# Optimization experiments

Hardware: AMD Instinct MI355X
Metric: run time of the kernel (lower is better)

Reference implementation:

```python
import jax, jax.numpy as jnp
import numpy as np

ALPHA = 0.2          # LeakyReLU negative slope
NEG_INF = -9.0e15    # padding value used by the torch code before softmax


def setup_inputs() -> dict:
    key = jax.random.key(0)
    k1, k2, k3, k4 = jax.random.split(key, 4)
    B, N, F_IN, F_OUT = 32, 1024, 128, 128
    # Dense 0/1 adjacency with self-loops (every node has degree >= 1)
    u = jax.random.uniform(k1, (B, N, N))
    adj = (u < 0.03).astype(jnp.float32)
    adj = jnp.maximum(adj, jnp.eye(N, dtype=jnp.float32)[None, :, :])
    batch_features = jax.random.normal(k2, (B, N, F_IN), dtype=jnp.float32)
    W = jax.random.normal(k3, (F_OUT, F_IN), dtype=jnp.float32) * 0.1  # nn.Linear weight [out,in]
    a = jax.random.normal(k4, (2 * F_OUT, 1), dtype=jnp.float32) * 0.1
    return {"batch_graphs": adj, "batch_features": batch_features, "W": W, "a": a}


def reference(batch_graphs, batch_features, W, a):
    # batch_graphs: [B,N,N] 0/1 adjacency; batch_features: [B,N,F_in]
    D = W.shape[0]
    h = jnp.einsum('bnf,df->bnd', batch_features, W)  # fc (no bias), dropout=0 is a no-op
    # score(i,j) = LeakyReLU(a[:D].h_i + a[D:].h_j); concat order is [center_i || neighbor_j]
    a_src = a[:D, 0]
    a_dst = a[D:, 0]
    s = h @ a_src                                   # [B,N] center term
    t = h @ a_dst                                   # [B,N] neighbor term
    scores = s[:, :, None] + t[:, None, :]          # [B,N,N]
    scores = jnp.where(scores > 0, scores, ALPHA * scores)
    # segmented softmax over each node's neighbors (pad_sequence with -9e15 == masked softmax)
    masked = jnp.where(batch_graphs == 1.0, scores, NEG_INF)
    attn = jax.nn.softmax(masked, axis=-1) * batch_graphs  # *adj zeros non-edges exactly (and deg-0 rows)
    # weighted sum of neighbor features scattered back to each node
    out = jnp.einsum('bij,bjd->bid', attn, h)       # [B,N,D]
    return out
```

## Files before the change

kernel.cpp:

```cpp
#include <hip/hip_runtime.h>
#include <hip/hip_bf16.h>

#define B_ 32
#define N_ 1024
#define F_ 128
#define ALPHA_ 0.2f
#define PSTR 72

typedef __attribute__((ext_vector_type(8))) short short8_t;
typedef __attribute__((ext_vector_type(4))) short short4_t;
typedef __attribute__((ext_vector_type(4))) float f32x4;

static __device__ __forceinline__ unsigned short bf16b(float f) {
    return __bfloat16_as_ushort(__float2bfloat16(f));
}

#define WAIT_VM2()  asm volatile("s_waitcnt vmcnt(2)" ::: "memory")
#define WAIT_VM0()  asm volatile("s_waitcnt vmcnt(0)" ::: "memory")
#define WAIT_LGKM() asm volatile("s_waitcnt lgkmcnt(0)" ::: "memory")
#define SCHEDB()    __builtin_amdgcn_sched_barrier(0)
#define BAR()       __builtin_amdgcn_s_barrier()

__global__ __launch_bounds__(256) void hst_kernel(
    const float* __restrict__ feat, const float* __restrict__ W,
    const float* __restrict__ a, float* __restrict__ h,
    float* __restrict__ s_out, float* __restrict__ t_out)
{
    __shared__ unsigned short Wt[128 * 128];
    __shared__ float fl[64 * 128];
    const int tid = threadIdx.x;
    const long row0 = (long)blockIdx.x * 64;

    for (int i = tid; i < 128 * 128; i += 256) {
        int d = i >> 7, k = i & 127;
        Wt[k * 128 + d] = bf16b(W[i]);
    }
    for (int i = tid; i < 64 * 128; i += 256) {
        int r = i >> 7, k = i & 127;
        fl[r * 128 + ((k + 8 * (r >> 2)) & 127)] = feat[(row0 + r) * 128 + k];
    }
    __syncthreads();

    const int oct = tid & 15;
    const int rg  = tid >> 4;
    const int d0  = oct * 8;
    const int r0  = rg * 4;

    float acc[4][8];
    #pragma unroll
    for (int q = 0; q < 4; ++q)
        #pragma unroll
        for (int c = 0; c < 8; ++c) acc[q][c] = 0.f;

    for (int kc = 0; kc < 128; kc += 4) {
        float wv[4][8];
        #pragma unroll
        for (int kk = 0; kk < 4; ++kk) {
            short8_t wr = *reinterpret_cast<const short8_t*>(&Wt[(kc + kk) * 128 + d0]);
            #pragma unroll
            for (int c = 0; c < 8; ++c) {
                union { unsigned u; float f; } cv;
                cv.u = ((unsigned)(unsigned short)wr[c]) << 16;
                wv[kk][c] = cv.f;
            }
        }
        #pragma unroll
        for (int q = 0; q < 4; ++q) {
            int r = r0 + q;
            int koff = (kc + 8 * (r >> 2)) & 127;
            float4 fv = *reinterpret_cast<const float4*>(&fl[r * 128 + koff]);
            float fq[4] = {fv.x, fv.y, fv.z, fv.w};
            #pragma unroll
            for (int kk = 0; kk < 4; ++kk)
                #pragma unroll
                for (int c = 0; c < 8; ++c)
                    acc[q][c] = fmaf(fq[kk], wv[kk][c], acc[q][c]);
        }
    }

    float asrc[8], adst[8];
    #pragma unroll
    for (int c = 0; c < 8; ++c) { asrc[c] = a[d0 + c]; adst[c] = a[128 + d0 + c]; }

    #pragma unroll
    for (int q = 0; q < 4; ++q) {
        long row = row0 + r0 + q;
        float4 h0 = make_float4(acc[q][0], acc[q][1], acc[q][2], acc[q][3]);
        float4 h1 = make_float4(acc[q][4], acc[q][5], acc[q][6], acc[q][7]);
        *reinterpret_cast<float4*>(&h[row * 128 + d0])     = h0;
        *reinterpret_cast<float4*>(&h[row * 128 + d0 + 4]) = h1;
        float sv = 0.f, tv = 0.f;
        #pragma unroll
        for (int c = 0; c < 8; ++c) {
            sv = fmaf(acc[q][c], asrc[c], sv);
            tv = fmaf(acc[q][c], adst[c], tv);
        }
        #pragma unroll
        for (int off = 1; off < 16; off <<= 1) {
            sv += __shfl_xor(sv, off);
            tv += __shfl_xor(tv, off);
        }
        if (oct == 0) { s_out[row] = sv; t_out[row] = tv; }
    }
}

__global__ __launch_bounds__(256) void tr_kernel(
    const float* __restrict__ h, unsigned short* __restrict__ hT)
{
    __shared__ unsigned short lt[128 * PSTR];
    const int tid = threadIdx.x;
    const int b   = blockIdx.x >> 4;
    const int j0  = (blockIdx.x & 15) * 64;

    const int j  = tid >> 2;
    const int dc = (tid & 3) * 4;
    const float* hr = h + ((size_t)(b * N_ + j0 + j)) * F_;
    #pragma unroll
    for (int q = 0; q < 8; ++q) {
        float4 v = *reinterpret_cast<const float4*>(hr + dc + q * 16);
        #pragma unroll
        for (int e = 0; e < 4; ++e)
            lt[(dc + q * 16 + e) * PSTR + j] = bf16b((&v.x)[e]);
    }
    __syncthreads();

    const int d    = tid >> 1;
    const int half = tid & 1;
    unsigned short* dst = hT + ((size_t)b * F_ + d) * N_ + j0 + half * 32;
    #pragma unroll
    for (int q = 0; q < 4; ++q)
        *reinterpret_cast<short8_t*>(dst + q * 8) =
            *reinterpret_cast<const short8_t*>(&lt[d * PSTR + half * 32 + q * 8]);
}

__global__ __launch_bounds__(512, 4) void attn4_kernel(
    const float* __restrict__ adj, const unsigned short* __restrict__ hT,
    const float* __restrict__ s_in, const float* __restrict__ t_in,
    float* __restrict__ out)
{
    __shared__ float adjb[2][64 * 64];
    __shared__ unsigned short ht[128 * PSTR];
    __shared__ unsigned short pt[64 * PSTR];
    __shared__ float tl[N_];
    __shared__ float sl[64], rsl[64];

    const int tid  = threadIdx.x;
    const int lane = tid & 63;
    const int w    = tid >> 6;

    const int blk = (blockIdx.x & 7) * 64 + (blockIdx.x >> 3);
    const int b   = blk >> 4;
    const int i0  = (blk & 15) * 64;

    tl[tid]       = t_in[b * N_ + tid];
    tl[tid + 512] = t_in[b * N_ + tid + 512];
    if (tid < 64) sl[tid] = s_in[b * N_ + i0 + tid];

    const int sr = w * 8 + (lane >> 4);
    const int sc = (lane & 15) * 4;
    const float* gsrc = adj + (size_t)(b * N_ + i0) * N_;

#define STAGE_ADJ(K, BUF) do {                                                 \
    __builtin_amdgcn_global_load_lds(                                          \
        (const __attribute__((address_space(1))) void*)                        \
            (gsrc + (size_t)sr * N_ + (K) * 64 + sc),                          \
        (__attribute__((address_space(3))) void*)&adjb[BUF][(w * 2 + 0) * 256],\
        16, 0, 0);                                                             \
    __builtin_amdgcn_global_load_lds(                                          \
        (const __attribute__((address_space(1))) void*)                        \
            (gsrc + (size_t)(sr + 4) * N_ + (K) * 64 + sc),                    \
        (__attribute__((address_space(3))) void*)&adjb[BUF][(w * 2 + 1) * 256],\
        16, 0, 0);                                                             \
} while (0)

    const unsigned short* hTb = hT + (size_t)b * F_ * N_;
    short8_t h_reg[2];
#define LOAD_H(K) do {                                                         \
    _Pragma("unroll")                                                          \
    for (int c = 0; c < 2; ++c) {                                              \
        int ch = tid + c * 512;                                                \
        h_reg[c] = *reinterpret_cast<const short8_t*>(                         \
            hTb + (size_t)(ch >> 3) * N_ + ((K) * 64 + (ch & 7) * 8));         \
    }                                                                          \
} while (0)

    const int gi = tid >> 3;
    const int gj = (tid & 7) * 8;
    const int m0 = (w >> 2) * 32;
    const int n0 = (w & 3) * 32;
    const int lm = tid & 15;
    const int kg = (tid & 63) >> 4;

    f32x4 acc[2][2];
    #pragma unroll
    for (int nf = 0; nf < 2; ++nf)
        #pragma unroll
        for (int mf = 0; mf < 2; ++mf) acc[nf][mf] = (f32x4){0.f, 0.f, 0.f, 0.f};
    float rs = 0.f;

    STAGE_ADJ(0, 0);
    LOAD_H(0);
    WAIT_VM2();
    WAIT_LGKM();
    SCHEDB();
    BAR();
    const float s_i = sl[gi];

    #pragma unroll
    for (int k = 0; k < 16; ++k) {
        const int cur = k & 1;
        if (k + 1 < 16) STAGE_ADJ(k + 1, cur ^ 1);
        #pragma unroll
        for (int c = 0; c < 2; ++c) {
            int ch = tid + c * 512;
            *reinterpret_cast<short8_t*>(&ht[(ch >> 3) * PSTR + (ch & 7) * 8]) = h_reg[c];
        }
        {
            float4 a0 = *reinterpret_cast<const float4*>(&adjb[cur][gi * 64 + gj]);
            float4 a1 = *reinterpret_cast<const float4*>(&adjb[cur][gi * 64 + gj + 4]);
            float4 t0 = *reinterpret_cast<const float4*>(&tl[k * 64 + gj]);
            float4 t1 = *reinterpret_cast<const float4*>(&tl[k * 64 + gj + 4]);
            short4_t pk0, pk1;
            #pragma unroll
            for (int e = 0; e < 4; ++e) {
                float sc0 = s_i + (&t0.x)[e];
                sc0 = fmaxf(sc0, ALPHA_ * sc0);
                float p = __expf(sc0) * (&a0.x)[e];
                rs += p;
                pk0[e] = (short)bf16b(p);
            }
            #pragma unroll
            for (int e = 0; e < 4; ++e) {
                float sc1 = s_i + (&t1.x)[e];
                sc1 = fmaxf(sc1, ALPHA_ * sc1);
                float p = __expf(sc1) * (&a1.x)[e];
                rs += p;
                pk1[e] = (short)bf16b(p);
            }
            *reinterpret_cast<short4_t*>(&pt[gi * PSTR + gj])     = pk0;
            *reinterpret_cast<short4_t*>(&pt[gi * PSTR + gj + 4]) = pk1;
        }
        if (k + 1 < 16) LOAD_H(k + 1);
        WAIT_LGKM();
        SCHEDB();
        BAR();
        #pragma unroll
        for (int ks = 0; ks < 2; ++ks) {
            short8_t b0 = *reinterpret_cast<const short8_t*>(
                &ht[(n0 + lm) * PSTR + ks * 32 + kg * 8]);
            short8_t b1 = *reinterpret_cast<const short8_t*>(
                &ht[(n0 + 16 + lm) * PSTR + ks * 32 + kg * 8]);
            short8_t a0f = *reinterpret_cast<const short8_t*>(
                &pt[(m0 + lm) * PSTR + ks * 32 + kg * 8]);
            short8_t a1f = *reinterpret_cast<const short8_t*>(
                &pt[(m0 + 16 + lm) * PSTR + ks * 32 + kg * 8]);
            acc[0][0] = __builtin_amdgcn_mfma_f32_16x16x32_bf16(a0f, b0, acc[0][0], 0, 0, 0);
            acc[1][0] = __builtin_amdgcn_mfma_f32_16x16x32_bf16(a0f, b1, acc[1][0], 0, 0, 0);
            acc[0][1] = __builtin_amdgcn_mfma_f32_16x16x32_bf16(a1f, b0, acc[0][1], 0, 0, 0);
            acc[1][1] = __builtin_amdgcn_mfma_f32_16x16x32_bf16(a1f, b1, acc[1][1], 0, 0, 0);
        }
        if (k + 1 < 16) { WAIT_VM2(); } else { WAIT_VM0(); }
        SCHEDB();
        BAR();
    }

    rs += __shfl_xor(rs, 1);
    rs += __shfl_xor(rs, 2);
    rs += __shfl_xor(rs, 4);
    if ((tid & 7) == 0) rsl[gi] = 1.0f / rs;
    __syncthreads();

    const int rbase = m0 + ((tid & 63) >> 4) * 4;
    float* ob = out + ((size_t)(b * N_ + i0)) * F_;
    #pragma unroll
    for (int mf = 0; mf < 2; ++mf) {
        f32x4 inv = *reinterpret_cast<const f32x4*>(&rsl[rbase + mf * 16]);
        #pragma unroll
        for (int r = 0; r < 4; ++r) {
            int row = rbase + mf * 16 + r;
            #pragma unroll
            for (int nf = 0; nf < 2; ++nf)
                ob[(size_t)row * F_ + n0 + nf * 16 + lm] = acc[nf][mf][r] * inv[r];
        }
    }
#undef STAGE_ADJ
#undef LOAD_H
}

extern "C" void kernel_launch(void* const* d_in, const int* in_sizes, int n_in,
                              void* d_out, int out_size, void* d_ws, size_t ws_size,
                              hipStream_t stream)
{
    const float* adj  = (const float*)d_in[0];
    const float* feat = (const float*)d_in[1];
    const float* W    = (const float*)d_in[2];
    const float* a    = (const float*)d_in[3];
    float* out = (float*)d_out;

    float* h = (float*)d_out;
    unsigned short* hT = (unsigned short*)d_ws;
    float* s = (float*)((char*)d_ws + (size_t)B_ * F_ * N_ * 2);
    float* t = s + (size_t)B_ * N_;

    hst_kernel<<<(B_ * N_) / 64, 256, 0, stream>>>(feat, W, a, h, s, t);
    tr_kernel<<<B_ * 16, 256, 0, stream>>>(h, hT);
    attn4_kernel<<<B_ * 16, 512, 0, stream>>>(adj, hT, s, t, out);
}
```

Before: 72.15 us.

## Fuse transpose into projection kernel and triple-buffer adjacency staging

The projection kernel now writes bf16 transposed h directly, so the separate transpose kernel and the fp32 h round trip through global memory go away. The attention kernel moves from double to triple buffering of adjacency tiles, issuing loads two tiles ahead and double-buffering the h register prefetch, with adjusted vmcnt waits. Adjacency loads use a cache-policy bit, and feature reads and output stores become nontemporal. Extra LDS for the third buffer may reduce occupancy, and the transposed stores from the projection kernel are narrow 8-byte writes.

```diff
diff --git a/kernel.cpp b/kernel.cpp
--- a/kernel.cpp
+++ b/kernel.cpp
@@ -15,6 +15,7 @@
     return __bfloat16_as_ushort(__float2bfloat16(f));
 }
 
+#define WAIT_VM4()  asm volatile("s_waitcnt vmcnt(4)" ::: "memory")
 #define WAIT_VM2()  asm volatile("s_waitcnt vmcnt(2)" ::: "memory")
 #define WAIT_VM0()  asm volatile("s_waitcnt vmcnt(0)" ::: "memory")
 #define WAIT_LGKM() asm volatile("s_waitcnt lgkmcnt(0)" ::: "memory")
@@ -23,13 +24,15 @@
 
 __global__ __launch_bounds__(256) void hst_kernel(
     const float* __restrict__ feat, const float* __restrict__ W,
-    const float* __restrict__ a, float* __restrict__ h,
+    const float* __restrict__ a, unsigned short* __restrict__ hT,
     float* __restrict__ s_out, float* __restrict__ t_out)
 {
     __shared__ unsigned short Wt[128 * 128];
     __shared__ float fl[64 * 128];
     const int tid = threadIdx.x;
     const long row0 = (long)blockIdx.x * 64;
+    const int b  = (int)(row0 >> 10);
+    const int jb = (int)(row0 & 1023);
 
     for (int i = tid; i < 128 * 128; i += 256) {
         int d = i >> 7, k = i & 127;
@@ -37,7 +40,8 @@
     }
     for (int i = tid; i < 64 * 128; i += 256) {
         int r = i >> 7, k = i & 127;
-        fl[r * 128 + ((k + 8 * (r >> 2)) & 127)] = feat[(row0 + r) * 128 + k];
+        fl[r * 128 + ((k + 8 * (r >> 2)) & 127)] =
+            __builtin_nontemporal_load(&feat[(row0 + r) * 128 + k]);
     }
     __syncthreads();
 
@@ -78,6 +82,15 @@
         }
     }
 
+    #pragma unroll
+    for (int c = 0; c < 8; ++c) {
+        short4_t hp;
+        #pragma unroll
+        for (int q = 0; q < 4; ++q) hp[q] = (short)bf16b(acc[q][c]);
+        *reinterpret_cast<short4_t*>(
+            &hT[((size_t)b * 128 + d0 + c) * 1024 + jb + r0]) = hp;
+    }
+
     float asrc[8], adst[8];
     #pragma unroll
     for (int c = 0; c < 8; ++c) { asrc[c] = a[d0 + c]; adst[c] = a[128 + d0 + c]; }
@@ -85,10 +98,6 @@
     #pragma unroll
     for (int q = 0; q < 4; ++q) {
         long row = row0 + r0 + q;
-        float4 h0 = make_float4(acc[q][0], acc[q][1], acc[q][2], acc[q][3]);
-        float4 h1 = make_float4(acc[q][4], acc[q][5], acc[q][6], acc[q][7]);
-        *reinterpret_cast<float4*>(&h[row * 128 + d0])     = h0;
-        *reinterpret_cast<float4*>(&h[row * 128 + d0 + 4]) = h1;
         float sv = 0.f, tv = 0.f;
         #pragma unroll
         for (int c = 0; c < 8; ++c) {
@@ -102,35 +111,6 @@
         }
         if (oct == 0) { s_out[row] = sv; t_out[row] = tv; }
     }
-}
-
-__global__ __launch_bounds__(256) void tr_kernel(
-    const float* __restrict__ h, unsigned short* __restrict__ hT)
-{
-    __shared__ unsigned short lt[128 * PSTR];
-    const int tid = threadIdx.x;
-    const int b   = blockIdx.x >> 4;
-    const int j0  = (blockIdx.x & 15) * 64;
-
-    const int j  = tid >> 2;
-    const int dc = (tid & 3) * 4;
-    const float* hr = h + ((size_t)(b * N_ + j0 + j)) * F_;
-    #pragma unroll
-    for (int q = 0; q < 8; ++q) {
-        float4 v = *reinterpret_cast<const float4*>(hr + dc + q * 16);
-        #pragma unroll
-        for (int e = 0; e < 4; ++e)
-            lt[(dc + q * 16 + e) * PSTR + j] = bf16b((&v.x)[e]);
-    }
-    __syncthreads();
-
-    const int d    = tid >> 1;
-    const int half = tid & 1;
-    unsigned short* dst = hT + ((size_t)b * F_ + d) * N_ + j0 + half * 32;
-    #pragma unroll
-    for (int q = 0; q < 4; ++q)
-        *reinterpret_cast<short8_t*>(dst + q * 8) =
-            *reinterpret_cast<const short8_t*>(&lt[d * PSTR + half * 32 + q * 8]);
 }
 
 __global__ __launch_bounds__(512, 4) void attn4_kernel(
@@ -138,7 +118,7 @@
     const float* __restrict__ s_in, const float* __restrict__ t_in,
     float* __restrict__ out)
 {
-    __shared__ float adjb[2][64 * 64];
+    __shared__ float adjb[3][64 * 64];
     __shared__ unsigned short ht[128 * PSTR];
     __shared__ unsigned short pt[64 * PSTR];
     __shared__ float tl[N_];
@@ -165,21 +145,21 @@
         (const __attribute__((address_space(1))) void*)                        \
             (gsrc + (size_t)sr * N_ + (K) * 64 + sc),                          \
         (__attribute__((address_space(3))) void*)&adjb[BUF][(w * 2 + 0) * 256],\
-        16, 0, 0);                                                             \
+        16, 0, 2 );                                                    \
     __builtin_amdgcn_global_load_lds(                                          \
         (const __attribute__((address_space(1))) void*)                        \
             (gsrc + (size_t)(sr + 4) * N_ + (K) * 64 + sc),                    \
         (__attribute__((address_space(3))) void*)&adjb[BUF][(w * 2 + 1) * 256],\
-        16, 0, 0);                                                             \
+        16, 0, 2 );                                                    \
 } while (0)
 
     const unsigned short* hTb = hT + (size_t)b * F_ * N_;
-    short8_t h_reg[2];
+    short8_t h_reg[2][2];
 #define LOAD_H(K) do {                                                         \
     _Pragma("unroll")                                                          \
     for (int c = 0; c < 2; ++c) {                                              \
         int ch = tid + c * 512;                                                \
-        h_reg[c] = *reinterpret_cast<const short8_t*>(                         \
+        h_reg[(K) & 1][c] = *reinterpret_cast<const short8_t*>(                \
             hTb + (size_t)(ch >> 3) * N_ + ((K) * 64 + (ch & 7) * 8));         \
     }                                                                          \
 } while (0)
@@ -200,7 +180,8 @@
 
     STAGE_ADJ(0, 0);
     LOAD_H(0);
-    WAIT_VM2();
+    STAGE_ADJ(1, 1);
+    WAIT_VM4();
     WAIT_LGKM();
     SCHEDB();
     BAR();
@@ -208,16 +189,18 @@
 
     #pragma unroll
     for (int k = 0; k < 16; ++k) {
-        const int cur = k & 1;
-        if (k + 1 < 16) STAGE_ADJ(k + 1, cur ^ 1);
+        if (k + 1 < 16) LOAD_H(k + 1);
+        if (k + 2 < 16) STAGE_ADJ(k + 2, (k + 2) % 3);
         #pragma unroll
         for (int c = 0; c < 2; ++c) {
             int ch = tid + c * 512;
-            *reinterpret_cast<short8_t*>(&ht[(ch >> 3) * PSTR + (ch & 7) * 8]) = h_reg[c];
+            *reinterpret_cast<short8_t*>(&ht[(ch >> 3) * PSTR + (ch & 7) * 8]) =
+                h_reg[k & 1][c];
         }
         {
-            float4 a0 = *reinterpret_cast<const float4*>(&adjb[cur][gi * 64 + gj]);
-            float4 a1 = *reinterpret_cast<const float4*>(&adjb[cur][gi * 64 + gj + 4]);
+            const float* ab = &adjb[k % 3][gi * 64 + gj];
+            float4 a0 = *reinterpret_cast<const float4*>(ab);
+            float4 a1 = *reinterpret_cast<const float4*>(ab + 4);
             float4 t0 = *reinterpret_cast<const float4*>(&tl[k * 64 + gj]);
             float4 t1 = *reinterpret_cast<const float4*>(&tl[k * 64 + gj + 4]);
             short4_t pk0, pk1;
@@ -240,7 +223,6 @@
             *reinterpret_cast<short4_t*>(&pt[gi * PSTR + gj])     = pk0;
             *reinterpret_cast<short4_t*>(&pt[gi * PSTR + gj + 4]) = pk1;
         }
-        if (k + 1 < 16) LOAD_H(k + 1);
         WAIT_LGKM();
         SCHEDB();
         BAR();
@@ -259,7 +241,9 @@
             acc[0][1] = __builtin_amdgcn_mfma_f32_16x16x32_bf16(a1f, b0, acc[0][1], 0, 0, 0);
             acc[1][1] = __builtin_amdgcn_mfma_f32_16x16x32_bf16(a1f, b1, acc[1][1], 0, 0, 0);
         }
-        if (k + 1 < 16) { WAIT_VM2(); } else { WAIT_VM0(); }
+        if (k + 2 < 16)      { WAIT_VM4(); }
+        else if (k + 1 < 16) { WAIT_VM2(); }
+        else                 { WAIT_VM0(); }
         SCHEDB();
         BAR();
     }
@@ -280,7 +264,9 @@
             int row = rbase + mf * 16 + r;
             #pragma unroll
             for (int nf = 0; nf < 2; ++nf)
-                ob[(size_t)row * F_ + n0 + nf * 16 + lm] = acc[nf][mf][r] * inv[r];
+                __builtin_nontemporal_store(
+                    acc[nf][mf][r] * inv[r],
+                    &ob[(size_t)row * F_ + n0 + nf * 16 + lm]);
         }
     }
 #undef STAGE_ADJ
@@ -297,12 +283,10 @@
     const float* a    = (const float*)d_in[3];
     float* out = (float*)d_out;
 
-    float* h = (float*)d_out;
     unsigned short* hT = (unsigned short*)d_ws;
     float* s = (float*)((char*)d_ws + (size_t)B_ * F_ * N_ * 2);
     float* t = s + (size_t)B_ * N_;
 
-    hst_kernel<<<(B_ * N_) / 64, 256, 0, stream>>>(feat, W, a, h, s, t);
-    tr_kernel<<<B_ * 16, 256, 0, stream>>>(h, hT);
+    hst_kernel<<<(B_ * N_) / 64, 256, 0, stream>>>(feat, W, a, hT, s, t);
     attn4_kernel<<<B_ * 16, 512, 0, stream>>>(adj, hT, s, t, out);
 }
```

New measurement: 87.30 us. 21.0% more time.
